# Kernel tuning notes

Hardware: AMD Instinct MI355X
Metric: run time of the kernel (lower is better)

## Reference

```python
import jax, jax.numpy as jnp
import numpy as np

B, N, IN_DIM, HID_DIM = 4, 256, 256, 128
H_SAT = W_SAT = 256
SEARCH_STEPS = 16


def _bilinear_sample(sim_map, px, py):
    # sim_map: [B,N,H,W]; px,py: [B,S,N] pixel coords (grid_sample align_corners=False convention, zeros padding)
    Bn, Nn, H, W = sim_map.shape
    x0 = jnp.floor(px); y0 = jnp.floor(py)
    x1 = x0 + 1.0;      y1 = y0 + 1.0
    wx1 = px - x0; wx0 = 1.0 - wx1
    wy1 = py - y0; wy0 = 1.0 - wy1
    b = jnp.arange(Bn)[:, None, None]
    n = jnp.arange(Nn)[None, None, :]
    def gather(xi, yi):
        valid = (xi >= 0) & (xi <= W - 1) & (yi >= 0) & (yi <= H - 1)
        xc = jnp.clip(xi, 0, W - 1).astype(jnp.int32)
        yc = jnp.clip(yi, 0, H - 1).astype(jnp.int32)
        v = sim_map[b, n, yc, xc]
        return jnp.where(valid, v, 0.0)
    return (wy0 * wx0 * gather(x0, y0) + wy0 * wx1 * gather(x1, y0)
            + wy1 * wx0 * gather(x0, y1) + wy1 * wx1 * gather(x1, y1))


def reference(node_coords, node_scores, node_features, node_depths, K_left,
              R_left2world, t_left2world_init, sat_featmap, K_sat, R_sat2world,
              t_sat2world, search_radius, search_steps, W_node, b_node, W_sat,
              b_sat, logit_scale):
    Bn, Nn, _ = node_features.shape
    nf = node_features @ W_node + b_node                                   # [B,N,C]
    sf = jnp.einsum('bchw,oc->bohw', sat_featmap, W_sat) + b_sat[None, :, None, None]
    _, C, H, W = sf.shape
    nf = nf / jnp.maximum(jnp.linalg.norm(nf, axis=-1, keepdims=True), 1e-12)
    sf = sf / jnp.maximum(jnp.linalg.norm(sf, axis=1, keepdims=True), 1e-12)
    sim_map = jnp.einsum('bnc,bchw->bnhw', nf, sf)                         # [B,N,H,W]

    step = jnp.linspace(-1.0, 1.0, search_steps)
    oy, ox = jnp.meshgrid(step, step, indexing='ij')
    offsets = jnp.stack([ox, oy], axis=-1).reshape(-1, 2)                  # [S,2]
    off2 = offsets[None] * search_radius.reshape(Bn, 1, 1)                 # [B,S,2]
    off3 = jnp.pad(off2, ((0, 0), (0, 0), (0, 1)))                         # z offset = 0
    cand_t = t_left2world_init[:, None, :] + off3                          # [B,S,3]

    # image2world: cam ray = K_left^-1 [u,v,1], scaled by depth, rotated + translated
    ones = jnp.ones((Bn, Nn, 1), nf.dtype)
    homog = jnp.concatenate([node_coords, ones], axis=-1)                  # [B,N,3]
    Kinv = jnp.linalg.inv(K_left)
    cam = jnp.einsum('bij,bnj->bni', Kinv, homog) * node_depths[..., None]
    worldR = jnp.einsum('bij,bnj->bni', R_left2world, cam)                 # [B,N,3]
    world = worldR[:, None] + cand_t[:, :, None]                           # [B,S,N,3]

    # world2image (satellite): cam = R^T (world - t), pixel = K cam / z
    cam_s = jnp.einsum('bji,bsnj->bsni', R_sat2world, world - t_sat2world[:, None, None, :])
    uvw = jnp.einsum('bij,bsnj->bsni', K_sat, cam_s)
    cand_coords = uvw[..., :2] / uvw[..., 2:3]                             # [B,S,N,2]

    scale = jnp.array([W - 1, H - 1], nf.dtype)
    nc = cand_coords / scale * 2.0 - 1.0
    px = ((nc[..., 0] + 1.0) * W - 1.0) * 0.5
    py = ((nc[..., 1] + 1.0) * H - 1.0) * 0.5
    sim_per_node = _bilinear_sample(sim_map, px, py)                       # [B,S,N]

    logits = jnp.sum(node_scores[:, None, :] * sim_per_node, axis=2)       # [B,S]
    scores = jax.nn.softmax(logits * jnp.exp(logit_scale), axis=1)
    best = jnp.argmax(scores, axis=1)                                      # [B]
    match = jnp.take_along_axis(cand_coords, best[:, None, None, None], axis=1)[:, 0]
    valid = ((match[..., 0] >= 0) & (match[..., 0] < W)
             & (match[..., 1] >= 0) & (match[..., 1] < H))
    return match, valid, cand_t, scores


def setup_inputs() -> dict:
    key = jax.random.key(0)
    ks = jax.random.split(key, 12)
    f32 = jnp.float32
    # realistic pinhole intrinsics; identity rotations
    K_left = jnp.tile(jnp.array([[400., 0., 128.], [0., 400., 128.], [0., 0., 1.]], f32), (B, 1, 1))
    K_sat = jnp.tile(jnp.array([[500., 0., 128.], [0., 500., 128.], [0., 0., 1.]], f32), (B, 1, 1))
    R_left2world = jnp.tile(jnp.eye(3, dtype=f32), (B, 1, 1))
    R_sat2world = jnp.tile(jnp.eye(3, dtype=f32), (B, 1, 1))
    t_left2world_init = jax.random.normal(ks[0], (B, 3), f32) * 2.0
    t_sat2world = jnp.tile(jnp.array([0., 0., -200.], f32), (B, 1))
    node_coords = jax.random.uniform(ks[1], (B, N, 2), f32) * 255.0
    node_depths = jax.random.uniform(ks[2], (B, N), f32) * 40.0 + 5.0
    node_scores = jax.random.uniform(ks[3], (B, N), f32)
    node_features = jax.random.normal(ks[4], (B, N, IN_DIM), f32)
    sat_featmap = jax.random.normal(ks[5], (B, IN_DIM, H_SAT, W_SAT), f32)
    search_radius = jax.random.uniform(ks[6], (B,), f32) * 5.0 + 5.0
    # parameters
    W_node = jax.random.normal(ks[7], (IN_DIM, HID_DIM), f32) / np.sqrt(IN_DIM)
    b_node = jnp.zeros((HID_DIM,), f32)
    W_sat = jax.random.normal(ks[8], (HID_DIM, IN_DIM), f32) / np.sqrt(IN_DIM)
    b_sat = jnp.zeros((HID_DIM,), f32)
    logit_scale = jnp.asarray(np.log(1.0 / 0.07), f32)
    return {
        'node_coords': node_coords, 'node_scores': node_scores,
        'node_features': node_features, 'node_depths': node_depths,
        'K_left': K_left, 'R_left2world': R_left2world,
        't_left2world_init': t_left2world_init, 'sat_featmap': sat_featmap,
        'K_sat': K_sat, 'R_sat2world': R_sat2world, 't_sat2world': t_sat2world,
        'search_radius': search_radius, 'search_steps': SEARCH_STEPS,
        'W_node': W_node, 'b_node': b_node, 'W_sat': W_sat, 'b_sat': b_sat,
        'logit_scale': logit_scale,
    }
```

## Files before the change

### kernel.cpp

```cpp
#include <hip/hip_runtime.h>
#include <stdint.h>

typedef _Float16 f16;
typedef __attribute__((ext_vector_type(8))) _Float16 f16x8;
typedef __attribute__((ext_vector_type(4))) _Float16 f16x4;
typedef __attribute__((ext_vector_type(4))) float    f32x4;

constexpr int BB   = 4;
constexpr int NN   = 256;
constexpr int CIN  = 256;
constexpr int CHID = 128;
constexpr int HH   = 256;
constexpr int WW   = 256;
constexpr int NPIX = HH * WW;
constexpr int SS   = 256;

constexpr int OUT_MATCH  = 0;
constexpr int OUT_VALID  = 2048;
constexpr int OUT_CANDT  = 3072;
constexpr int OUT_SCORES = 6144;

static __device__ __forceinline__ void compute_geom(
    const float* Kl, const float* Rl, const float* ti,
    const float* Ks, const float* Rs, const float* ts,
    float u, float v, float d, float* A, float* ub)
{
  float a = Kl[0], bq = Kl[1], c = Kl[2];
  float dq = Kl[3], e = Kl[4], f = Kl[5];
  float g = Kl[6], h = Kl[7], i = Kl[8];
  float cof00 =  (e*i - f*h), cof01 = -(dq*i - f*g), cof02 =  (dq*h - e*g);
  float cof10 = -(bq*i - c*h), cof11 =  (a*i - c*g), cof12 = -(a*h - bq*g);
  float cof20 =  (bq*f - c*e), cof21 = -(a*f - c*dq), cof22 =  (a*e - bq*dq);
  float det = a*cof00 + bq*cof01 + c*cof02;
  float inv = 1.0f / det;
  float k00 = cof00*inv, k01 = cof10*inv, k02 = cof20*inv;
  float k10 = cof01*inv, k11 = cof11*inv, k12 = cof21*inv;
  float k20 = cof02*inv, k21 = cof12*inv, k22 = cof22*inv;
  float cx = (k00*u + k01*v + k02) * d;
  float cy = (k10*u + k11*v + k12) * d;
  float cz = (k20*u + k21*v + k22) * d;
  float w0 = Rl[0]*cx + Rl[1]*cy + Rl[2]*cz + ti[0] - ts[0];
  float w1 = Rl[3]*cx + Rl[4]*cy + Rl[5]*cz + ti[1] - ts[1];
  float w2 = Rl[6]*cx + Rl[7]*cy + Rl[8]*cz + ti[2] - ts[2];
  #pragma unroll
  for (int r = 0; r < 3; ++r)
    #pragma unroll
    for (int cJ = 0; cJ < 3; ++cJ)
      A[r*3 + cJ] = Ks[r*3+0]*Rs[cJ*3+0] + Ks[r*3+1]*Rs[cJ*3+1] + Ks[r*3+2]*Rs[cJ*3+2];
  ub[0] = A[0]*w0 + A[1]*w1 + A[2]*w2;
  ub[1] = A[3]*w0 + A[4]*w1 + A[5]*w2;
  ub[2] = A[6]*w0 + A[7]*w1 + A[8]*w2;
}

static __device__ __forceinline__ void proj(const float* A, const float* ub,
                                            float oxr, float oyr,
                                            float& cx, float& cy)
{
  float u0 = ub[0] + oxr*A[0] + oyr*A[1];
  float u1 = ub[1] + oxr*A[3] + oyr*A[4];
  float u2 = ub[2] + oxr*A[6] + oyr*A[7];
  cx = u0 / u2;
  cy = u1 / u2;
}


__global__ __launch_bounds__(256) void kPrep(const float* __restrict__ Wsat,
                                             f16* __restrict__ Wh,
                                             f16* __restrict__ Wl,
                                             float* __restrict__ logits)
{
  int idx = blockIdx.x * 256 + threadIdx.x;
  float v = Wsat[idx];
  f16 hv = (f16)v;
  Wh[idx] = hv;
  Wl[idx] = (f16)(v - (float)hv);
  if (idx < BB*SS) logits[idx] = 0.0f;
}

__global__ __launch_bounds__(128) void kNode(const float* __restrict__ feats,
                                             const float* __restrict__ Wn,
                                             const float* __restrict__ bn,
                                             float* __restrict__ nf)
{
  int bnI = blockIdx.x;
  int h = threadIdx.x;
  __shared__ float frow[CIN];
  __shared__ float red[2];
  frow[h]       = feats[(size_t)bnI*CIN + h];
  frow[h + 128] = feats[(size_t)bnI*CIN + h + 128];
  __syncthreads();
  float acc = bn[h];
  #pragma unroll 8
  for (int c = 0; c < CIN; ++c) acc += frow[c] * Wn[c*CHID + h];
  float s = acc * acc;
  #pragma unroll
  for (int off = 32; off; off >>= 1) s += __shfl_down(s, off);
  if ((h & 63) == 0) red[h >> 6] = s;
  __syncthreads();
  float inv = 1.0f / fmaxf(sqrtf(red[0] + red[1]), 1e-12f);
  nf[(size_t)bnI*CHID + h] = acc * inv;
}

constexpr int PITCH = 264;

__global__ __launch_bounds__(256, 2) void kSatM(
    const float* __restrict__ sat, const f16* __restrict__ Wh,
    const f16* __restrict__ Wl, const float* __restrict__ bsat,
    f16* __restrict__ sfn)
{
  const int b  = blockIdx.y;
  const int p0 = blockIdx.x * 64;
  __shared__ f16 FhS[64 * PITCH];
  __shared__ f16 FlS[64 * PITCH];
  __shared__ float nrm[4][64];

  const int tid = threadIdx.x;
  const int w   = tid >> 6;
  const int l   = tid & 63;

  {
    const int q  = tid & 15;
    const int cg = tid >> 4;
    const float* Fb = sat + (size_t)b * CIN * NPIX + p0;
    #pragma unroll
    for (int pass = 0; pass < 4; ++pass) {
      int cbase = pass * 64 + cg * 4;
      float4 r0 = *(const float4*)(Fb + (size_t)(cbase + 0) * NPIX + q*4);
      float4 r1 = *(const float4*)(Fb + (size_t)(cbase + 1) * NPIX + q*4);
      float4 r2 = *(const float4*)(Fb + (size_t)(cbase + 2) * NPIX + q*4);
      float4 r3 = *(const float4*)(Fb + (size_t)(cbase + 3) * NPIX + q*4);
      float pv[4][4] = {{r0.x,r1.x,r2.x,r3.x},{r0.y,r1.y,r2.y,r3.y},
                        {r0.z,r1.z,r2.z,r3.z},{r0.w,r1.w,r2.w,r3.w}};
      #pragma unroll
      for (int i2 = 0; i2 < 4; ++i2) {
        f16x4 hv, lv;
        #pragma unroll
        for (int j = 0; j < 4; ++j) {
          float v = pv[i2][j];
          f16 hq = (f16)v;
          hv[j] = hq;
          lv[j] = (f16)(v - (float)hq);
        }
        *(f16x4*)(FhS + (q*4 + i2)*PITCH + cbase) = hv;
        *(f16x4*)(FlS + (q*4 + i2)*PITCH + cbase) = lv;
      }
    }
  }

  f16x8 wah[2][8], wal[2][8];
  {
    int orow = w*32 + (l & 15);
    int kofs = (l >> 4) * 8;
    #pragma unroll
    for (int ot = 0; ot < 2; ++ot) {
      const f16* bh = Wh + (size_t)(orow + ot*16) * CIN + kofs;
      const f16* blp = Wl + (size_t)(orow + ot*16) * CIN + kofs;
      #pragma unroll
      for (int ks = 0; ks < 8; ++ks) {
        wah[ot][ks] = *(const f16x8*)(bh + ks*32);
        wal[ot][ks] = *(const f16x8*)(blp + ks*32);
      }
    }
  }

  f32x4 acc[4][2];
  {
    int ob = w*32 + (l >> 4) * 4;
    f32x4 b0 = *(const f32x4*)(bsat + ob);
    f32x4 b1 = *(const f32x4*)(bsat + ob + 16);
    #pragma unroll
    for (int pt = 0; pt < 4; ++pt) { acc[pt][0] = b0; acc[pt][1] = b1; }
  }

  __syncthreads();

  #pragma unroll
  for (int ks = 0; ks < 8; ++ks) {
    #pragma unroll
    for (int pt = 0; pt < 4; ++pt) {
      int rofs = (pt*16 + (l & 15)) * PITCH + ks*32 + (l >> 4) * 8;
      f16x8 bh = *(const f16x8*)(FhS + rofs);
      f16x8 bl = *(const f16x8*)(FlS + rofs);
      #pragma unroll
      for (int ot = 0; ot < 2; ++ot) {
        acc[pt][ot] = __builtin_amdgcn_mfma_f32_16x16x32_f16(wah[ot][ks], bh, acc[pt][ot], 0, 0, 0);
        acc[pt][ot] = __builtin_amdgcn_mfma_f32_16x16x32_f16(wah[ot][ks], bl, acc[pt][ot], 0, 0, 0);
        acc[pt][ot] = __builtin_amdgcn_mfma_f32_16x16x32_f16(wal[ot][ks], bh, acc[pt][ot], 0, 0, 0);
      }
    }
  }

  #pragma unroll
  for (int pt = 0; pt < 4; ++pt) {
    float s = 0.0f;
    #pragma unroll
    for (int ot = 0; ot < 2; ++ot)
      #pragma unroll
      for (int r = 0; r < 4; ++r) s += acc[pt][ot][r] * acc[pt][ot][r];
    s += __shfl_xor(s, 16);
    s += __shfl_xor(s, 32);
    if ((l >> 4) == 0) nrm[w][pt*16 + l] = s;
  }
  __syncthreads();

  #pragma unroll
  for (int pt = 0; pt < 4; ++pt) {
    int p = pt*16 + (l & 15);
    float n2 = nrm[0][p] + nrm[1][p] + nrm[2][p] + nrm[3][p];
    float invn = 1.0f / fmaxf(sqrtf(n2), 1e-12f);
    size_t rowb = ((size_t)b*NPIX + p0 + p) * CHID + w*32 + (l >> 4) * 4;
    #pragma unroll
    for (int ot = 0; ot < 2; ++ot) {
      f16x4 o4;
      #pragma unroll
      for (int r = 0; r < 4; ++r) o4[r] = (f16)(acc[pt][ot][r] * invn);
      *(f16x4*)(sfn + rowb + ot*16) = o4;
    }
  }
}

__global__ __launch_bounds__(256) void kSampleH(
    const f16* __restrict__ sfn, const float* __restrict__ nf,
    const float* __restrict__ node_coords, const float* __restrict__ node_scores,
    const float* __restrict__ node_depths,
    const float* __restrict__ Kl, const float* __restrict__ Rl,
    const float* __restrict__ tinit, const float* __restrict__ Ks,
    const float* __restrict__ Rs, const float* __restrict__ tsat,
    const float* __restrict__ radius, float* __restrict__ logits)
{
  int bnI = blockIdx.x;
  int b = bnI >> 8;
  int tid = threadIdx.x;
  __shared__ uint32_t cpk[SS];
  __shared__ float4   cwt[SS];
  __shared__ float    simbuf[SS];

  {
    float A[9], ub[3];
    compute_geom(Kl + b*9, Rl + b*9, tinit + b*3, Ks + b*9, Rs + b*9, tsat + b*3,
                 node_coords[bnI*2 + 0], node_coords[bnI*2 + 1], node_depths[bnI],
                 A, ub);
    float rad = radius[b];
    int s = tid;
    int sx = s & 15, sy = s >> 4;
    float oxr = (-1.0f + sx*(2.0f/15.0f)) * rad;
    float oyr = (-1.0f + sy*(2.0f/15.0f)) * rad;
    float cx, cy;
    proj(A, ub, oxr, oyr, cx, cy);
    float px = cx * (256.0f/255.0f) - 0.5f;
    float py = cy * (256.0f/255.0f) - 0.5f;
    float x0f = floorf(px), y0f = floorf(py);
    float wx1 = px - x0f, wy1 = py - y0f;
    float wx0 = 1.0f - wx1, wy0 = 1.0f - wy1;
    int x0 = (int)x0f, y0 = (int)y0f;
    int x1 = x0 + 1, y1 = y0 + 1;
    bool vx0 = (x0 >= 0) && (x0 < WW);
    bool vx1 = (x1 >= 0) && (x1 < WW);
    bool vy0 = (y0 >= 0) && (y0 < HH);
    bool vy1 = (y1 >= 0) && (y1 < HH);
    int x0c = min(max(x0, 0), WW-1), x1c = min(max(x1, 0), WW-1);
    int y0c = min(max(y0, 0), HH-1), y1c = min(max(y1, 0), HH-1);
    cpk[s] = (uint32_t)x0c | ((uint32_t)x1c << 8)
           | ((uint32_t)y0c << 16) | ((uint32_t)y1c << 24);
    float4 wv;
    wv.x = (vx0 && vy0) ? wy0*wx0 : 0.0f;
    wv.y = (vx1 && vy0) ? wy0*wx1 : 0.0f;
    wv.z = (vx0 && vy1) ? wy1*wx0 : 0.0f;
    wv.w = (vx1 && vy1) ? wy1*wx1 : 0.0f;
    cwt[s] = wv;
  }

  const int l    = tid & 63;
  const int w    = tid >> 6;
  const int cg   = l & 31;
  const int half = l >> 5;
  const int c4   = cg * 4;
  f32x4 nf4 = *(const f32x4*)(nf + (size_t)bnI*CHID + c4);
  const f16* __restrict__ base = sfn + (size_t)b * NPIX * CHID;

  __syncthreads();

  #pragma unroll 4
  for (int it = 0; it < 32; ++it) {
    int s = it*8 + w*2 + half;
    uint32_t pc = cpk[s];
    float4 wt = cwt[s];
    int x0c = pc & 255, x1c = (pc >> 8) & 255;
    int r0 = ((pc >> 16) & 255) << 8;
    int r1 = (pc >> 24) << 8;
    f16x4 v00 = *(const f16x4*)(base + (((r0 + x0c) << 7) + c4));
    f16x4 v10 = *(const f16x4*)(base + (((r0 + x1c) << 7) + c4));
    f16x4 v01 = *(const f16x4*)(base + (((r1 + x0c) << 7) + c4));
    f16x4 v11 = *(const f16x4*)(base + (((r1 + x1c) << 7) + c4));
    float d00 = nf4[0]*(float)v00[0] + nf4[1]*(float)v00[1]
              + nf4[2]*(float)v00[2] + nf4[3]*(float)v00[3];
    float d10 = nf4[0]*(float)v10[0] + nf4[1]*(float)v10[1]
              + nf4[2]*(float)v10[2] + nf4[3]*(float)v10[3];
    float d01 = nf4[0]*(float)v01[0] + nf4[1]*(float)v01[1]
              + nf4[2]*(float)v01[2] + nf4[3]*(float)v01[3];
    float d11 = nf4[0]*(float)v11[0] + nf4[1]*(float)v11[1]
              + nf4[2]*(float)v11[2] + nf4[3]*(float)v11[3];
    float p = wt.x*d00 + wt.y*d10 + wt.z*d01 + wt.w*d11;
    #pragma unroll
    for (int off = 1; off < 32; off <<= 1) p += __shfl_xor(p, off);
    if (cg == 0) simbuf[s] = p;
  }
  __syncthreads();

  atomicAdd(&logits[b*SS + tid], node_scores[bnI] * simbuf[tid]);
}


__global__ __launch_bounds__(256) void kZero(float* stash)
{
  int idx = blockIdx.x * 256 + threadIdx.x;
  if (idx < BB*SS) stash[idx] = 0.0f;
}

__global__ __launch_bounds__(256) void kDirectSlow(
    const float* __restrict__ sat, const float* __restrict__ Wsat,
    const float* __restrict__ bsat, const float* __restrict__ feats,
    const float* __restrict__ Wn, const float* __restrict__ bn,
    const float* __restrict__ node_coords, const float* __restrict__ node_scores,
    const float* __restrict__ node_depths,
    const float* __restrict__ Kl, const float* __restrict__ Rl,
    const float* __restrict__ tinit, const float* __restrict__ Ks,
    const float* __restrict__ Rs, const float* __restrict__ tsat,
    const float* __restrict__ radius, float* logitsStash)
{
  __shared__ float frow[CIN];
  __shared__ float nfs[CHID];
  __shared__ float satc[4][CIN];
  __shared__ float sfb[4][256];
  __shared__ float red[8];

  int bnI = blockIdx.x;
  int b = bnI >> 8;
  int tid = threadIdx.x;
  int lane = tid & 63, wv = tid >> 6;

  frow[tid] = feats[(size_t)bnI*CIN + tid];
  __syncthreads();

  {
    float acc = 0.0f;
    if (tid < CHID) {
      acc = bn[tid];
      for (int c = 0; c < CIN; ++c) acc += frow[c] * Wn[c*CHID + tid];
    }
    float s2 = (tid < CHID) ? acc*acc : 0.0f;
    #pragma unroll
    for (int off = 32; off; off >>= 1) s2 += __shfl_down(s2, off);
    if (lane == 0) red[wv] = s2;
    __syncthreads();
    float inv = 1.0f / fmaxf(sqrtf(red[0] + red[1] + red[2] + red[3]), 1e-12f);
    if (tid < CHID) nfs[tid] = acc * inv;
    __syncthreads();
  }

  float A[9], ub[3];
  compute_geom(Kl + b*9, Rl + b*9, tinit + b*3, Ks + b*9, Rs + b*9, tsat + b*3,
               node_coords[bnI*2 + 0], node_coords[bnI*2 + 1], node_depths[bnI],
               A, ub);
  float rad = radius[b];
  float score_n = node_scores[bnI];
  const int h = tid & 127, half = tid >> 7;
  const float* Wrow = Wsat + (size_t)h * CIN + half * 128;

  for (int s = 0; s < SS; ++s) {
    int sx = s & 15, sy = s >> 4;
    float oxr = (-1.0f + sx*(2.0f/15.0f)) * rad;
    float oyr = (-1.0f + sy*(2.0f/15.0f)) * rad;
    float cx, cy;
    proj(A, ub, oxr, oyr, cx, cy);
    float px = cx * (256.0f/255.0f) - 0.5f;
    float py = cy * (256.0f/255.0f) - 0.5f;
    float x0f = floorf(px), y0f = floorf(py);
    float wx1 = px - x0f, wy1 = py - y0f;
    float wx0 = 1.0f - wx1, wy0 = 1.0f - wy1;
    int x0 = (int)x0f, y0 = (int)y0f, x1 = x0 + 1, y1 = y0 + 1;
    int cxs[4] = {x0, x1, x0, x1};
    int cys[4] = {y0, y0, y1, y1};
    float wts[4] = {wy0*wx0, wy0*wx1, wy1*wx0, wy1*wx1};
    #pragma unroll
    for (int j = 0; j < 4; ++j) {
      bool ok = (cxs[j] >= 0) && (cxs[j] < WW) && (cys[j] >= 0) && (cys[j] < HH);
      if (!ok) wts[j] = 0.0f;
      cxs[j] = min(max(cxs[j], 0), WW - 1);
      cys[j] = min(max(cys[j], 0), HH - 1);
    }
    __syncthreads();
    {
      size_t base = (size_t)(b*CIN + tid) * NPIX;
      #pragma unroll
      for (int j = 0; j < 4; ++j)
        satc[j][tid] = sat[base + cys[j]*WW + cxs[j]];
    }
    __syncthreads();
    {
      float a0 = 0.f, a1 = 0.f, a2 = 0.f, a3 = 0.f;
      #pragma unroll 4
      for (int k = 0; k < 128; k += 4) {
        float4 w = *(const float4*)(Wrow + k);
        int kk = half*128 + k;
        a0 += w.x*satc[0][kk] + w.y*satc[0][kk+1] + w.z*satc[0][kk+2] + w.w*satc[0][kk+3];
        a1 += w.x*satc[1][kk] + w.y*satc[1][kk+1] + w.z*satc[1][kk+2] + w.w*satc[1][kk+3];
        a2 += w.x*satc[2][kk] + w.y*satc[2][kk+1] + w.z*satc[2][kk+2] + w.w*satc[2][kk+3];
        a3 += w.x*satc[3][kk] + w.y*satc[3][kk+1] + w.z*satc[3][kk+2] + w.w*satc[3][kk+3];
      }
      sfb[0][tid] = a0; sfb[1][tid] = a1; sfb[2][tid] = a2; sfb[3][tid] = a3;
    }
    __syncthreads();
    float samp = 0.0f;
    #pragma unroll 1
    for (int j = 0; j < 4; ++j) {
      float n2 = 0.0f, nd = 0.0f;
      if (tid < CHID) {
        float sfh = sfb[j][tid] + sfb[j][tid + 128] + bsat[tid];
        n2 = sfh * sfh;
        nd = nfs[tid] * sfh;
      }
      #pragma unroll
      for (int off = 32; off; off >>= 1) {
        n2 += __shfl_down(n2, off);
        nd += __shfl_down(nd, off);
      }
      if (lane == 0) { red[wv*2] = n2; red[wv*2 + 1] = nd; }
      __syncthreads();
      float t1 = red[0] + red[2] + red[4] + red[6];
      float t2 = red[1] + red[3] + red[5] + red[7];
      samp += wts[j] * (t2 / fmaxf(sqrtf(t1), 1e-12f));
      __syncthreads();
    }
    if (tid == 0) atomicAdd(&logitsStash[b*SS + s], score_n * samp);
  }
}


__global__ __launch_bounds__(256) void kFinal(
    const float* logits, const float* lscale,
    const float* radius, const float* tinit,
    const float* node_coords, const float* node_depths,
    const float* Kl, const float* Rl,
    const float* Ks, const float* Rs,
    const float* tsat, float* out)
{
  int b = blockIdx.x;
  int tid = threadIdx.x;
  int lane = tid & 63, wv = tid >> 6;
  __shared__ float redm[4], rede[4], av[4];
  __shared__ int ai[4], bestS;

  float scale = expf(lscale[0]);
  float t = logits[b*SS + tid] * scale;

  float m = t;
  #pragma unroll
  for (int off = 32; off; off >>= 1) m = fmaxf(m, __shfl_down(m, off));
  if (lane == 0) redm[wv] = m;
  __syncthreads();
  float M = fmaxf(fmaxf(redm[0], redm[1]), fmaxf(redm[2], redm[3]));

  float e = expf(t - M);
  float se = e;
  #pragma unroll
  for (int off = 32; off; off >>= 1) se += __shfl_down(se, off);
  if (lane == 0) rede[wv] = se;
  __syncthreads();
  float Z = rede[0] + rede[1] + rede[2] + rede[3];

  float vmax = t; int idx = tid;
  #pragma unroll
  for (int off = 32; off; off >>= 1) {
    float ov = __shfl_down(vmax, off);
    int   oi = __shfl_down(idx, off);
    if (ov > vmax || (ov == vmax && oi < idx)) { vmax = ov; idx = oi; }
  }
  if (lane == 0) { av[wv] = vmax; ai[wv] = idx; }
  __syncthreads();
  if (tid == 0) {
    float bv = av[0]; int bi = ai[0];
    #pragma unroll
    for (int w = 1; w < 4; ++w)
      if (av[w] > bv || (av[w] == bv && ai[w] < bi)) { bv = av[w]; bi = ai[w]; }
    bestS = bi;
  }
  __syncthreads();
  int best = bestS;

  out[OUT_SCORES + b*SS + tid] = e / Z;

  float rad = radius[b];
  {
    int sx = tid & 15, sy = tid >> 4;
    float ox = -1.0f + sx*(2.0f/15.0f);
    float oy = -1.0f + sy*(2.0f/15.0f);
    size_t ct = OUT_CANDT + ((size_t)b*SS + tid)*3;
    out[ct + 0] = tinit[b*3 + 0] + ox*rad;
    out[ct + 1] = tinit[b*3 + 1] + oy*rad;
    out[ct + 2] = tinit[b*3 + 2];
  }

  {
    int n = tid;
    int bnI = b*NN + n;
    float A[9], ub[3];
    compute_geom(Kl + b*9, Rl + b*9, tinit + b*3, Ks + b*9, Rs + b*9, tsat + b*3,
                 node_coords[bnI*2 + 0], node_coords[bnI*2 + 1], node_depths[bnI],
                 A, ub);
    int bx = best & 15, by = best >> 4;
    float oxr = (-1.0f + bx*(2.0f/15.0f)) * rad;
    float oyr = (-1.0f + by*(2.0f/15.0f)) * rad;
    float cx, cy;
    proj(A, ub, oxr, oyr, cx, cy);
    out[OUT_MATCH + (size_t)bnI*2 + 0] = cx;
    out[OUT_MATCH + (size_t)bnI*2 + 1] = cy;
    float vl = (cx >= 0.0f && cx < (float)WW && cy >= 0.0f && cy < (float)HH) ? 1.0f : 0.0f;
    out[OUT_VALID + bnI] = vl;
  }
}

extern "C" void kernel_launch(void* const* d_in, const int* in_sizes, int n_in,
                              void* d_out, int out_size, void* d_ws, size_t ws_size,
                              hipStream_t stream)
{
  (void)in_sizes; (void)n_in; (void)out_size;
  const float* node_coords   = (const float*)d_in[0];
  const float* node_scores   = (const float*)d_in[1];
  const float* node_features = (const float*)d_in[2];
  const float* node_depths   = (const float*)d_in[3];
  const float* K_left        = (const float*)d_in[4];
  const float* R_l2w         = (const float*)d_in[5];
  const float* t_init        = (const float*)d_in[6];
  const float* sat           = (const float*)d_in[7];
  const float* K_sat         = (const float*)d_in[8];
  const float* R_sat         = (const float*)d_in[9];
  const float* t_sat         = (const float*)d_in[10];
  const float* radius        = (const float*)d_in[11];
  const float* W_node        = (const float*)d_in[13];
  const float* b_node        = (const float*)d_in[14];
  const float* W_sat         = (const float*)d_in[15];
  const float* b_sat         = (const float*)d_in[16];
  const float* lscale        = (const float*)d_in[17];

  float* out = (float*)d_out;
  char* ws = (char*)d_ws;

  const size_t sfnB = (size_t)BB * NPIX * CHID * sizeof(f16);
  const size_t whB  = (size_t)CIN * CHID * sizeof(f16);
  const size_t nfB  = (size_t)BB * NN * CHID * sizeof(float);
  const size_t logB = (size_t)BB * SS * sizeof(float);
  const size_t needA = sfnB + 2*whB + nfB + logB;

  if (ws_size >= needA) {
    f16*   sfn    = (f16*)ws;
    f16*   Wh     = (f16*)(ws + sfnB);
    f16*   Wl     = (f16*)(ws + sfnB + whB);
    float* nf     = (float*)(ws + sfnB + 2*whB);
    float* logits = (float*)(ws + sfnB + 2*whB + nfB);

    kPrep<<<128, 256, 0, stream>>>(W_sat, Wh, Wl, logits);
    kNode<<<BB*NN, 128, 0, stream>>>(node_features, W_node, b_node, nf);
    kSatM<<<dim3(NPIX/64, BB), 256, 0, stream>>>(sat, Wh, Wl, b_sat, sfn);
    kSampleH<<<BB*NN, 256, 0, stream>>>(sfn, nf, node_coords, node_scores,
        node_depths, K_left, R_l2w, t_init, K_sat, R_sat, t_sat, radius, logits);
    kFinal<<<BB, 256, 0, stream>>>(logits, lscale, radius, t_init, node_coords,
                                   node_depths, K_left, R_l2w, K_sat, R_sat,
                                   t_sat, out);
  } else {
    float* stash = out + OUT_SCORES;
    kZero<<<4, 256, 0, stream>>>(stash);
    kDirectSlow<<<BB*NN, 256, 0, stream>>>(sat, W_sat, b_sat, node_features,
        W_node, b_node, node_coords, node_scores, node_depths,
        K_left, R_l2w, t_init, K_sat, R_sat, t_sat, radius, stash);
    kFinal<<<BB, 256, 0, stream>>>(stash, lscale, radius, t_init, node_coords,
                                   node_depths, K_left, R_l2w, K_sat, R_sat,
                                   t_sat, out);
  }
}
```

Measured before the change: 479.7 us.

## Split satellite projection K loop into two halves with prefetch and smaller LDS

The satellite-feature projection kernel now processes the 256 input channels in two halves of 128. It stages each half through a smaller shared buffer and prefetches the second half's global loads into registers while the first half's MFMAs run. Halving LDS and weight registers allows raising launch bounds to 3 blocks per CU, aiming for higher occupancy and better latency hiding. This costs an extra barrier round and register pressure from the prefetch buffer.

```diff
diff --git a/kernel.cpp b/kernel.cpp
--- a/kernel.cpp
+++ b/kernel.cpp
@@ -101,67 +101,28 @@
   nf[(size_t)bnI*CHID + h] = acc * inv;
 }
 
-constexpr int PITCH = 264;
-
-__global__ __launch_bounds__(256, 2) void kSatM(
+constexpr int P2 = 136;
+
+__global__ __launch_bounds__(256, 3) void kSatM(
     const float* __restrict__ sat, const f16* __restrict__ Wh,
     const f16* __restrict__ Wl, const float* __restrict__ bsat,
     f16* __restrict__ sfn)
 {
   const int b  = blockIdx.y;
   const int p0 = blockIdx.x * 64;
-  __shared__ f16 FhS[64 * PITCH];
-  __shared__ f16 FlS[64 * PITCH];
+  __shared__ f16 FhS[64 * P2];
+  __shared__ f16 FlS[64 * P2];
   __shared__ float nrm[4][64];
 
   const int tid = threadIdx.x;
   const int w   = tid >> 6;
   const int l   = tid & 63;
-
-  {
-    const int q  = tid & 15;
-    const int cg = tid >> 4;
-    const float* Fb = sat + (size_t)b * CIN * NPIX + p0;
-    #pragma unroll
-    for (int pass = 0; pass < 4; ++pass) {
-      int cbase = pass * 64 + cg * 4;
-      float4 r0 = *(const float4*)(Fb + (size_t)(cbase + 0) * NPIX + q*4);
-      float4 r1 = *(const float4*)(Fb + (size_t)(cbase + 1) * NPIX + q*4);
-      float4 r2 = *(const float4*)(Fb + (size_t)(cbase + 2) * NPIX + q*4);
-      float4 r3 = *(const float4*)(Fb + (size_t)(cbase + 3) * NPIX + q*4);
-      float pv[4][4] = {{r0.x,r1.x,r2.x,r3.x},{r0.y,r1.y,r2.y,r3.y},
-                        {r0.z,r1.z,r2.z,r3.z},{r0.w,r1.w,r2.w,r3.w}};
-      #pragma unroll
-      for (int i2 = 0; i2 < 4; ++i2) {
-        f16x4 hv, lv;
-        #pragma unroll
-        for (int j = 0; j < 4; ++j) {
-          float v = pv[i2][j];
-          f16 hq = (f16)v;
-          hv[j] = hq;
-          lv[j] = (f16)(v - (float)hq);
-        }
-        *(f16x4*)(FhS + (q*4 + i2)*PITCH + cbase) = hv;
-        *(f16x4*)(FlS + (q*4 + i2)*PITCH + cbase) = lv;
-      }
-    }
-  }
-
-  f16x8 wah[2][8], wal[2][8];
-  {
-    int orow = w*32 + (l & 15);
-    int kofs = (l >> 4) * 8;
-    #pragma unroll
-    for (int ot = 0; ot < 2; ++ot) {
-      const f16* bh = Wh + (size_t)(orow + ot*16) * CIN + kofs;
-      const f16* blp = Wl + (size_t)(orow + ot*16) * CIN + kofs;
-      #pragma unroll
-      for (int ks = 0; ks < 8; ++ks) {
-        wah[ot][ks] = *(const f16x8*)(bh + ks*32);
-        wal[ot][ks] = *(const f16x8*)(blp + ks*32);
-      }
-    }
-  }
+  const int q   = tid & 15;
+  const int cg  = tid >> 4;
+  const float* Fb = sat + (size_t)b * CIN * NPIX + p0;
+
+  const int orow = w*32 + (l & 15);
+  const int koff = (l >> 4) * 8;
 
   f32x4 acc[4][2];
   {
@@ -172,13 +133,56 @@
     for (int pt = 0; pt < 4; ++pt) { acc[pt][0] = b0; acc[pt][1] = b1; }
   }
 
-  __syncthreads();
-
-  #pragma unroll
-  for (int ks = 0; ks < 8; ++ks) {
+  float4 r[8];
+  #pragma unroll
+  for (int p = 0; p < 2; ++p)
+    #pragma unroll
+    for (int j = 0; j < 4; ++j)
+      r[p*4 + j] = *(const float4*)(Fb + (size_t)(p*64 + cg*4 + j) * NPIX + q*4);
+
+  #pragma unroll
+  for (int p = 0; p < 2; ++p) {
+    int cbase = p*64 + cg*4;
+    #pragma unroll
+    for (int i2 = 0; i2 < 4; ++i2) {
+      f16x4 hv, lv;
+      #pragma unroll
+      for (int j = 0; j < 4; ++j) {
+        float v = (i2 == 0) ? r[p*4+j].x : (i2 == 1) ? r[p*4+j].y
+                : (i2 == 2) ? r[p*4+j].z : r[p*4+j].w;
+        f16 hq = (f16)v;
+        hv[j] = hq;
+        lv[j] = (f16)(v - (float)hq);
+      }
+      *(f16x4*)(FhS + (q*4 + i2)*P2 + cbase) = hv;
+      *(f16x4*)(FlS + (q*4 + i2)*P2 + cbase) = lv;
+    }
+  }
+  __syncthreads();
+
+  #pragma unroll
+  for (int p = 0; p < 2; ++p)
+    #pragma unroll
+    for (int j = 0; j < 4; ++j)
+      r[p*4 + j] = *(const float4*)(Fb + (size_t)(128 + p*64 + cg*4 + j) * NPIX + q*4);
+
+  f16x8 wah[2][4], wal[2][4];
+  #pragma unroll
+  for (int ot = 0; ot < 2; ++ot) {
+    const f16* bh  = Wh + (size_t)(orow + ot*16) * CIN + koff;
+    const f16* blp = Wl + (size_t)(orow + ot*16) * CIN + koff;
+    #pragma unroll
+    for (int ks = 0; ks < 4; ++ks) {
+      wah[ot][ks] = *(const f16x8*)(bh  + ks*32);
+      wal[ot][ks] = *(const f16x8*)(blp + ks*32);
+    }
+  }
+
+  #pragma unroll
+  for (int ks = 0; ks < 4; ++ks) {
     #pragma unroll
     for (int pt = 0; pt < 4; ++pt) {
-      int rofs = (pt*16 + (l & 15)) * PITCH + ks*32 + (l >> 4) * 8;
+      int rofs = (pt*16 + (l & 15)) * P2 + ks*32 + koff;
       f16x8 bh = *(const f16x8*)(FhS + rofs);
       f16x8 bl = *(const f16x8*)(FlS + rofs);
       #pragma unroll
@@ -189,6 +193,54 @@
       }
     }
   }
+  __syncthreads();
+
+  #pragma unroll
+  for (int p = 0; p < 2; ++p) {
+    int cbase = p*64 + cg*4;
+    #pragma unroll
+    for (int i2 = 0; i2 < 4; ++i2) {
+      f16x4 hv, lv;
+      #pragma unroll
+      for (int j = 0; j < 4; ++j) {
+        float v = (i2 == 0) ? r[p*4+j].x : (i2 == 1) ? r[p*4+j].y
+                : (i2 == 2) ? r[p*4+j].z : r[p*4+j].w;
+        f16 hq = (f16)v;
+        hv[j] = hq;
+        lv[j] = (f16)(v - (float)hq);
+      }
+      *(f16x4*)(FhS + (q*4 + i2)*P2 + cbase) = hv;
+      *(f16x4*)(FlS + (q*4 + i2)*P2 + cbase) = lv;
+    }
+  }
+
+  #pragma unroll
+  for (int ot = 0; ot < 2; ++ot) {
+    const f16* bh  = Wh + (size_t)(orow + ot*16) * CIN + 128 + koff;
+    const f16* blp = Wl + (size_t)(orow + ot*16) * CIN + 128 + koff;
+    #pragma unroll
+    for (int ks = 0; ks < 4; ++ks) {
+      wah[ot][ks] = *(const f16x8*)(bh  + ks*32);
+      wal[ot][ks] = *(const f16x8*)(blp + ks*32);
+    }
+  }
+  __syncthreads();
+
+  #pragma unroll
+  for (int ks = 0; ks < 4; ++ks) {
+    #pragma unroll
+    for (int pt = 0; pt < 4; ++pt) {
+      int rofs = (pt*16 + (l & 15)) * P2 + ks*32 + koff;
+      f16x8 bh = *(const f16x8*)(FhS + rofs);
+      f16x8 bl = *(const f16x8*)(FlS + rofs);
+      #pragma unroll
+      for (int ot = 0; ot < 2; ++ot) {
+        acc[pt][ot] = __builtin_amdgcn_mfma_f32_16x16x32_f16(wah[ot][ks], bh, acc[pt][ot], 0, 0, 0);
+        acc[pt][ot] = __builtin_amdgcn_mfma_f32_16x16x32_f16(wah[ot][ks], bl, acc[pt][ot], 0, 0, 0);
+        acc[pt][ot] = __builtin_amdgcn_mfma_f32_16x16x32_f16(wal[ot][ks], bh, acc[pt][ot], 0, 0, 0);
+      }
+    }
+  }
 
   #pragma unroll
   for (int pt = 0; pt < 4; ++pt) {
@@ -196,7 +248,7 @@
     #pragma unroll
     for (int ot = 0; ot < 2; ++ot)
       #pragma unroll
-      for (int r = 0; r < 4; ++r) s += acc[pt][ot][r] * acc[pt][ot][r];
+      for (int rr = 0; rr < 4; ++rr) s += acc[pt][ot][rr] * acc[pt][ot][rr];
     s += __shfl_xor(s, 16);
     s += __shfl_xor(s, 32);
     if ((l >> 4) == 0) nrm[w][pt*16 + l] = s;
@@ -213,7 +265,7 @@
     for (int ot = 0; ot < 2; ++ot) {
       f16x4 o4;
       #pragma unroll
-      for (int r = 0; r < 4; ++r) o4[r] = (f16)(acc[pt][ot][r] * invn);
+      for (int rr = 0; rr < 4; ++rr) o4[rr] = (f16)(acc[pt][ot][rr] * invn);
       *(f16x4*)(sfn + rowb + ot*16) = o4;
     }
   }
```

Result: no change. 482.8 us (+0.6%).

## Double-buffer channel chunks in satellite projection kernel with larger pixel tiles

Applied to the files above, without the earlier changes.

The satellite feature projection kernel now handles 128 pixels per block instead of 64 and streams the 256 input channels in four 64-channel chunks. It uses double-buffered LDS, loading the next chunk into registers while MFMAs run on the current one. This is meant to overlap global loads of the large feature map with the split-fp16 matrix multiply and to reuse each weight fragment across more pixels. In exchange it doubles the accumulator registers and adds extra barriers per chunk, which may reduce occupancy under the two-blocks-per-CU launch bound.

```diff
diff --git a/kernel.cpp b/kernel.cpp
--- a/kernel.cpp
+++ b/kernel.cpp
@@ -101,7 +101,29 @@
   nf[(size_t)bnI*CHID + h] = acc * inv;
 }
 
-constexpr int PITCH = 264;
+constexpr int P3   = 72;
+constexpr int HALF = 128 * P3;
+
+static __device__ __forceinline__ void cvt_write(f16* __restrict__ FhS,
+                                                 f16* __restrict__ FlS,
+                                                 int bufbase, int q, int cr,
+                                                 const float4* r)
+{
+  #pragma unroll
+  for (int i2 = 0; i2 < 4; ++i2) {
+    f16x8 hv, lv;
+    #pragma unroll
+    for (int j = 0; j < 8; ++j) {
+      float v = (i2 == 0) ? r[j].x : (i2 == 1) ? r[j].y
+              : (i2 == 2) ? r[j].z : r[j].w;
+      f16 hq = (f16)v;
+      hv[j] = hq;
+      lv[j] = (f16)(v - (float)hq);
+    }
+    *(f16x8*)(FhS + bufbase + (q*4 + i2)*P3 + cr*8) = hv;
+    *(f16x8*)(FlS + bufbase + (q*4 + i2)*P3 + cr*8) = lv;
+  }
+}
 
 __global__ __launch_bounds__(256, 2) void kSatM(
     const float* __restrict__ sat, const f16* __restrict__ Wh,
@@ -109,94 +131,85 @@
     f16* __restrict__ sfn)
 {
   const int b  = blockIdx.y;
-  const int p0 = blockIdx.x * 64;
-  __shared__ f16 FhS[64 * PITCH];
-  __shared__ f16 FlS[64 * PITCH];
-  __shared__ float nrm[4][64];
+  const int p0 = blockIdx.x * 128;
+  __shared__ f16 FhS[2 * HALF];
+  __shared__ f16 FlS[2 * HALF];
+  __shared__ float nrm[4][128];
 
   const int tid = threadIdx.x;
   const int w   = tid >> 6;
   const int l   = tid & 63;
-
-  {
-    const int q  = tid & 15;
-    const int cg = tid >> 4;
-    const float* Fb = sat + (size_t)b * CIN * NPIX + p0;
-    #pragma unroll
-    for (int pass = 0; pass < 4; ++pass) {
-      int cbase = pass * 64 + cg * 4;
-      float4 r0 = *(const float4*)(Fb + (size_t)(cbase + 0) * NPIX + q*4);
-      float4 r1 = *(const float4*)(Fb + (size_t)(cbase + 1) * NPIX + q*4);
-      float4 r2 = *(const float4*)(Fb + (size_t)(cbase + 2) * NPIX + q*4);
-      float4 r3 = *(const float4*)(Fb + (size_t)(cbase + 3) * NPIX + q*4);
-      float pv[4][4] = {{r0.x,r1.x,r2.x,r3.x},{r0.y,r1.y,r2.y,r3.y},
-                        {r0.z,r1.z,r2.z,r3.z},{r0.w,r1.w,r2.w,r3.w}};
-      #pragma unroll
-      for (int i2 = 0; i2 < 4; ++i2) {
-        f16x4 hv, lv;
-        #pragma unroll
-        for (int j = 0; j < 4; ++j) {
-          float v = pv[i2][j];
-          f16 hq = (f16)v;
-          hv[j] = hq;
-          lv[j] = (f16)(v - (float)hq);
-        }
-        *(f16x4*)(FhS + (q*4 + i2)*PITCH + cbase) = hv;
-        *(f16x4*)(FlS + (q*4 + i2)*PITCH + cbase) = lv;
+  const int q   = tid & 31;
+  const int cr  = tid >> 5;
+  const float* Fb = sat + (size_t)b * CIN * NPIX + p0;
+
+  const int orow = w*32 + (l & 15);
+  const int koff = (l >> 4) * 8;
+
+  f16x8 wah[4][2][2], wal[4][2][2];
+  #pragma unroll
+  for (int ph = 0; ph < 4; ++ph)
+    #pragma unroll
+    for (int ks = 0; ks < 2; ++ks)
+      #pragma unroll
+      for (int ot = 0; ot < 2; ++ot) {
+        wah[ph][ks][ot] = *(const f16x8*)(Wh + (size_t)(orow + ot*16)*CIN + ph*64 + ks*32 + koff);
+        wal[ph][ks][ot] = *(const f16x8*)(Wl + (size_t)(orow + ot*16)*CIN + ph*64 + ks*32 + koff);
       }
-    }
-  }
-
-  f16x8 wah[2][8], wal[2][8];
-  {
-    int orow = w*32 + (l & 15);
-    int kofs = (l >> 4) * 8;
-    #pragma unroll
-    for (int ot = 0; ot < 2; ++ot) {
-      const f16* bh = Wh + (size_t)(orow + ot*16) * CIN + kofs;
-      const f16* blp = Wl + (size_t)(orow + ot*16) * CIN + kofs;
-      #pragma unroll
-      for (int ks = 0; ks < 8; ++ks) {
-        wah[ot][ks] = *(const f16x8*)(bh + ks*32);
-        wal[ot][ks] = *(const f16x8*)(blp + ks*32);
-      }
-    }
-  }
-
-  f32x4 acc[4][2];
+
+  f32x4 acc[8][2];
   {
     int ob = w*32 + (l >> 4) * 4;
     f32x4 b0 = *(const f32x4*)(bsat + ob);
     f32x4 b1 = *(const f32x4*)(bsat + ob + 16);
     #pragma unroll
-    for (int pt = 0; pt < 4; ++pt) { acc[pt][0] = b0; acc[pt][1] = b1; }
-  }
-
-  __syncthreads();
-
-  #pragma unroll
-  for (int ks = 0; ks < 8; ++ks) {
-    #pragma unroll
-    for (int pt = 0; pt < 4; ++pt) {
-      int rofs = (pt*16 + (l & 15)) * PITCH + ks*32 + (l >> 4) * 8;
-      f16x8 bh = *(const f16x8*)(FhS + rofs);
-      f16x8 bl = *(const f16x8*)(FlS + rofs);
-      #pragma unroll
-      for (int ot = 0; ot < 2; ++ot) {
-        acc[pt][ot] = __builtin_amdgcn_mfma_f32_16x16x32_f16(wah[ot][ks], bh, acc[pt][ot], 0, 0, 0);
-        acc[pt][ot] = __builtin_amdgcn_mfma_f32_16x16x32_f16(wah[ot][ks], bl, acc[pt][ot], 0, 0, 0);
-        acc[pt][ot] = __builtin_amdgcn_mfma_f32_16x16x32_f16(wal[ot][ks], bh, acc[pt][ot], 0, 0, 0);
+    for (int pt = 0; pt < 8; ++pt) { acc[pt][0] = b0; acc[pt][1] = b1; }
+  }
+
+  float4 rA[8];
+  #pragma unroll
+  for (int j = 0; j < 8; ++j)
+    rA[j] = *(const float4*)(Fb + (size_t)(cr*8 + j) * NPIX + q*4);
+  cvt_write(FhS, FlS, 0, q, cr, rA);
+  __syncthreads();
+
+  #pragma unroll
+  for (int p = 0; p < 4; ++p) {
+    const int rb = (p & 1) * HALF;
+    if (p < 3) {
+      #pragma unroll
+      for (int j = 0; j < 8; ++j)
+        rA[j] = *(const float4*)(Fb + (size_t)((p+1)*64 + cr*8 + j) * NPIX + q*4);
+    }
+    #pragma unroll
+    for (int ks = 0; ks < 2; ++ks) {
+      #pragma unroll
+      for (int pt = 0; pt < 8; ++pt) {
+        int rofs = rb + (pt*16 + (l & 15)) * P3 + ks*32 + koff;
+        f16x8 bh = *(const f16x8*)(FhS + rofs);
+        f16x8 bl = *(const f16x8*)(FlS + rofs);
+        #pragma unroll
+        for (int ot = 0; ot < 2; ++ot) {
+          acc[pt][ot] = __builtin_amdgcn_mfma_f32_16x16x32_f16(wah[p][ks][ot], bh, acc[pt][ot], 0, 0, 0);
+          acc[pt][ot] = __builtin_amdgcn_mfma_f32_16x16x32_f16(wah[p][ks][ot], bl, acc[pt][ot], 0, 0, 0);
+          acc[pt][ot] = __builtin_amdgcn_mfma_f32_16x16x32_f16(wal[p][ks][ot], bh, acc[pt][ot], 0, 0, 0);
+        }
       }
     }
-  }
-
-  #pragma unroll
-  for (int pt = 0; pt < 4; ++pt) {
+    __syncthreads();
+    if (p < 3) {
+      cvt_write(FhS, FlS, ((p+1) & 1) * HALF, q, cr, rA);
+      __syncthreads();
+    }
+  }
+
+  #pragma unroll
+  for (int pt = 0; pt < 8; ++pt) {
     float s = 0.0f;
     #pragma unroll
     for (int ot = 0; ot < 2; ++ot)
       #pragma unroll
-      for (int r = 0; r < 4; ++r) s += acc[pt][ot][r] * acc[pt][ot][r];
+      for (int rr = 0; rr < 4; ++rr) s += acc[pt][ot][rr] * acc[pt][ot][rr];
     s += __shfl_xor(s, 16);
     s += __shfl_xor(s, 32);
     if ((l >> 4) == 0) nrm[w][pt*16 + l] = s;
@@ -204,7 +217,7 @@
   __syncthreads();
 
   #pragma unroll
-  for (int pt = 0; pt < 4; ++pt) {
+  for (int pt = 0; pt < 8; ++pt) {
     int p = pt*16 + (l & 15);
     float n2 = nrm[0][p] + nrm[1][p] + nrm[2][p] + nrm[3][p];
     float invn = 1.0f / fmaxf(sqrtf(n2), 1e-12f);
@@ -213,7 +226,7 @@
     for (int ot = 0; ot < 2; ++ot) {
       f16x4 o4;
       #pragma unroll
-      for (int r = 0; r < 4; ++r) o4[r] = (f16)(acc[pt][ot][r] * invn);
+      for (int rr = 0; rr < 4; ++rr) o4[rr] = (f16)(acc[pt][ot][rr] * invn);
       *(f16x4*)(sfn + rowb + ot*16) = o4;
     }
   }
@@ -561,7 +574,7 @@
 
     kPrep<<<128, 256, 0, stream>>>(W_sat, Wh, Wl, logits);
     kNode<<<BB*NN, 128, 0, stream>>>(node_features, W_node, b_node, nf);
-    kSatM<<<dim3(NPIX/64, BB), 256, 0, stream>>>(sat, Wh, Wl, b_sat, sfn);
+    kSatM<<<dim3(NPIX/128, BB), 256, 0, stream>>>(sat, Wh, Wl, b_sat, sfn);
     kSampleH<<<BB*NN, 256, 0, stream>>>(sfn, nf, node_coords, node_scores,
         node_depths, K_left, R_l2w, t_init, K_sat, R_sat, t_sat, radius, logits);
     kFinal<<<BB, 256, 0, stream>>>(logits, lscale, radius, t_init, node_coords,
```

New measurement: 472.2 us. About the same (-1.6%).
